# Performance work log

Measured on AMD Instinct MI355X. Metric: run time of the kernel, lower is better.

Reference implementation:

```python
import jax, jax.numpy as jnp
import numpy as np

F0, F1 = 10, 10  # num_neighbor_list fanouts
B = 4096         # sampled pos+neg edges


def setup_inputs() -> dict:
    key = jax.random.key(0)
    ks = jax.random.split(key, 24)
    def rn(k, shp, scale=0.05):
        return (jax.random.normal(k, shp, dtype=jnp.float32) * scale)
    inp = {
        "user_feat": rn(ks[0], (50000, 512), 1.0),
        "item_feat": rn(ks[1], (100000, 512), 1.0),
        "W_pu": rn(ks[2], (512, 256)), "b_pu": jnp.zeros((256,), jnp.float32),
        "W_pi": rn(ks[3], (512, 256)), "b_pi": jnp.zeros((256,), jnp.float32),
        "u_self0": rn(ks[4], (256, 256)), "u_agg0": rn(ks[5], (256, 256)),
        "u_self1": rn(ks[6], (256, 128)), "u_agg1": rn(ks[7], (256, 128)),
        "i_self0": rn(ks[8], (256, 256)), "i_agg0": rn(ks[9], (256, 256)),
        "i_self1": rn(ks[10], (256, 128)), "i_agg1": rn(ks[11], (256, 128)),
        "W_lin": rn(ks[12], (128, 1)), "b_lin": jnp.zeros((1,), jnp.float32),
        # precomputed multi-hop sampled node ids (alternating user/item spaces)
        "src_h0": jax.random.randint(ks[13], (B,), 0, 50000, dtype=jnp.int32),
        "src_h1": jax.random.randint(ks[14], (B * F0,), 0, 100000, dtype=jnp.int32),
        "src_h2": jax.random.randint(ks[15], (B * F0 * F1,), 0, 50000, dtype=jnp.int32),
        "dst_h0": jax.random.randint(ks[16], (B,), 0, 100000, dtype=jnp.int32),
        "dst_h1": jax.random.randint(ks[17], (B * F0,), 0, 50000, dtype=jnp.int32),
        "dst_h2": jax.random.randint(ks[18], (B * F0 * F1,), 0, 100000, dtype=jnp.int32),
    }
    return inp


def _sage(h0, h1, h2, Wself0, Wagg0, Wself1, Wagg1):
    # 2-layer GraphSAGE with mean aggregation over fixed fanouts.
    d = h0.shape[-1]
    # layer 0: update hop-0 and hop-1 representations
    n0 = h1.reshape(h0.shape[0], F0, d).mean(axis=1)          # [B, d]
    g0 = jax.nn.relu(h0 @ Wself0 + n0 @ Wagg0)                # [B, H0]
    n1 = h2.reshape(h1.shape[0], F1, d).mean(axis=1)          # [B*F0, d]
    g1 = jax.nn.relu(h1 @ Wself0 + n1 @ Wagg0)                # [B*F0, H0]
    # layer 1: final hop-0 representation (no activation on last layer)
    n = g1.reshape(g0.shape[0], F0, -1).mean(axis=1)          # [B, H0]
    return g0 @ Wself1 + n @ Wagg1                            # [B, H1]


def reference(user_feat, item_feat, W_pu, b_pu, W_pi, b_pi,
              u_self0, u_agg0, u_self1, u_agg1,
              i_self0, i_agg0, i_self1, i_agg1,
              W_lin, b_lin,
              src_h0, src_h1, src_h2, dst_h0, dst_h1, dst_h2):
    u_proj = jax.nn.sigmoid(user_feat @ W_pu + b_pu)   # [U, P]
    i_proj = jax.nn.sigmoid(item_feat @ W_pi + b_pi)   # [I, P]
    # src side alternates user/item per hop; dst side alternates item/user
    user_h = _sage(u_proj[src_h0], i_proj[src_h1], u_proj[src_h2],
                   u_self0, u_agg0, u_self1, u_agg1)
    item_h = _sage(i_proj[dst_h0], u_proj[dst_h1], i_proj[dst_h2],
                   i_self0, i_agg0, i_self1, i_agg1)
    logits = (user_h * item_h) @ W_lin + b_lin          # [B, 1]
    return logits
```

## Files before the change

kernel.cpp:

```cpp
#include <hip/hip_runtime.h>
#include <hip/hip_bf16.h>
#include <type_traits>

typedef __attribute__((ext_vector_type(8))) short short8;
typedef __attribute__((ext_vector_type(4))) float f32x4;
typedef unsigned short u16;
typedef unsigned int u32;

typedef const __attribute__((address_space(1))) u32* gp1_t;
typedef __attribute__((address_space(3))) u32* lp3_t;

__device__ __forceinline__ float bf2f(u16 u) {
    union { unsigned int i; float f; } x; x.i = ((unsigned int)u) << 16; return x.f;
}
__device__ __forceinline__ u16 f2bf(float f) {
    union { __hip_bfloat16 h; u16 u; } c; c.h = __float2bfloat16(f); return c.u;
}
__device__ __forceinline__ short8 cvt8(float4 v0, float4 v1) {
    union { u16 u[8]; short8 s; } p;
    p.u[0] = f2bf(v0.x); p.u[1] = f2bf(v0.y); p.u[2] = f2bf(v0.z); p.u[3] = f2bf(v0.w);
    p.u[4] = f2bf(v1.x); p.u[5] = f2bf(v1.y); p.u[6] = f2bf(v1.z); p.u[7] = f2bf(v1.w);
    return p.s;
}
__device__ __forceinline__ void gload_lds16(const void* g, void* l) {
    __builtin_amdgcn_global_load_lds((gp1_t)g, (lp3_t)l, 16, 0, 0);
}

struct TCJobs {
    const float* A[6];
    const float* Bm[6];
    u16* out[6];
    int N[6];
    int Ka[6];
};

__global__ void transcat6_k(TCJobs j) {
    int jid = blockIdx.y;
    int i = blockIdx.x * 256 + threadIdx.x;
    int N = j.N[jid];
    if (i >= N * 512) return;
    int n = i >> 9, k = i & 511, Ka = j.Ka[jid];
    float v = (k < Ka) ? j.A[jid][k * N + n] : j.Bm[jid][(k - Ka) * N + n];
    j.out[jid][i] = f2bf(v);
}

struct GJob {
    const void* A;
    const u16* WT;
    const float* bias;
    void* C;
    int M;
    int toff;
};
struct GJobs4 { GJob j[4]; };

template <int NJ, int WC, bool F32A, int ACT, bool OF32>
__global__ __launch_bounds__(WC * 128, 4) void gemm_k(GJobs4 js) {
    const int K = 512;
    const int N = WC * 64;
    __shared__ __align__(1024) char As[F32A ? 16384 : 8192];
    __shared__ __align__(1024) char Bs[WC * 4096];
    const int t = threadIdx.x;
    const int lane = t & 63;
    const int wid = t >> 6;
    const int wr = wid / WC, wc = wid % WC;
    const int lr = lane & 15;

    const int nwg = gridDim.x, p = blockIdx.x;
    const int q = nwg >> 3, rr = nwg & 7;
    const int xcd = p & 7, idx = p >> 3;
    const int L = (xcd < rr ? xcd * (q + 1) : rr * (q + 1) + (xcd - rr) * q) + idx;

    GJob jb = js.j[0];
    #pragma unroll
    for (int k = 1; k < NJ; ++k) if (L >= js.j[k].toff) jb = js.j[k];
    const int row_base = (L - jb.toff) * 128;
    const int M = jb.M;

    f32x4 acc[4][4] = {};

    for (int kt = 0; kt < K; kt += 32) {
        #pragma unroll
        for (int i = 0; i < 2; ++i) {
            int slot = wid * 2 + i;
            int rl = slot * 16 + (lane >> 2);
            int cc = (lane & 3) ^ ((rl >> 1) & 3);
            gload_lds16(&jb.WT[(size_t)rl * K + kt + cc * 8], &Bs[slot * 1024]);
        }
        if constexpr (F32A) {
            #pragma unroll
            for (int i = 0; i < 16 / (2 * WC); ++i) {
                int slot = wid * (16 / (2 * WC)) + i;
                int rl = slot * 8 + (lane >> 3);
                int sc = (lane & 7) ^ (rl & 7);
                int gr = row_base + rl; if (gr >= M) gr = M - 1;
                gload_lds16(&((const float*)jb.A)[(size_t)gr * K + kt + sc * 4],
                            &As[slot * 1024]);
            }
        } else {
            #pragma unroll
            for (int i = 0; i < 8 / (2 * WC); ++i) {
                int slot = wid * (8 / (2 * WC)) + i;
                int rl = slot * 16 + (lane >> 2);
                int cc = (lane & 3) ^ ((rl >> 1) & 3);
                int gr = row_base + rl; if (gr >= M) gr = M - 1;
                gload_lds16(&((const u16*)jb.A)[(size_t)gr * K + kt + cc * 8],
                            &As[slot * 1024]);
            }
        }
        __syncthreads();

        {
            const int g = lane >> 4;
            short8 a[4], b[4];
            #pragma unroll
            for (int ni = 0; ni < 4; ++ni) {
                int r = wc * 64 + ni * 16 + lr;
                b[ni] = *(const short8*)&Bs[r * 64 + ((g ^ ((r >> 1) & 3)) * 16)];
            }
            #pragma unroll
            for (int mi = 0; mi < 4; ++mi) {
                int r = wr * 64 + mi * 16 + lr;
                if constexpr (F32A) {
                    float4 v0 = *(const float4*)&As[r * 128 + (((2 * g) ^ (r & 7)) * 16)];
                    float4 v1 = *(const float4*)&As[r * 128 + (((2 * g + 1) ^ (r & 7)) * 16)];
                    a[mi] = cvt8(v0, v1);
                } else {
                    a[mi] = *(const short8*)&As[r * 64 + ((g ^ ((r >> 1) & 3)) * 16)];
                }
            }
            #pragma unroll
            for (int mi = 0; mi < 4; ++mi)
                #pragma unroll
                for (int ni = 0; ni < 4; ++ni)
                    acc[mi][ni] = __builtin_amdgcn_mfma_f32_16x16x32_bf16(
                        a[mi], b[ni], acc[mi][ni], 0, 0, 0);
        }
        __syncthreads();
    }

    #pragma unroll
    for (int mi = 0; mi < 4; ++mi) {
        int row0 = row_base + wr * 64 + mi * 16 + ((lane >> 4) << 2);
        #pragma unroll
        for (int ni = 0; ni < 4; ++ni) {
            int col = wc * 64 + ni * 16 + lr;
            float bv = jb.bias ? jb.bias[col] : 0.f;
            #pragma unroll
            for (int r = 0; r < 4; ++r) {
                int row = row0 + r;
                if (row < M) {
                    float x = acc[mi][ni][r] + bv;
                    if (ACT == 1) x = fmaxf(x, 0.f);
                    if (ACT == 2) x = 1.f / (1.f + __expf(-x));
                    if constexpr (OF32)
                        ((float*)jb.C)[(size_t)row * N + col] = x;
                    else
                        ((u16*)jb.C)[(size_t)row * N + col] = f2bf(x);
                }
            }
        }
    }
}

struct FJob {
    const u16* G0;
    const u16* G1;
    const u16* WT;
    float* C;
    int toff;
};
struct FJobs2 { FJob j[2]; };

__global__ __launch_bounds__(256, 4) void final_k(FJobs2 js) {
    const int K = 512;
    __shared__ __align__(1024) char As[8192];
    __shared__ __align__(1024) char Bs[8192];
    const int t = threadIdx.x;
    const int lane = t & 63;
    const int wid = t >> 6;
    const int wr = wid >> 1, wc = wid & 1;
    const int lr = lane & 15;

    const int L = blockIdx.x;
    FJob jb = js.j[0];
    if (L >= js.j[1].toff) jb = js.j[1];
    const int row_base = (L - jb.toff) * 128;

    f32x4 acc[4][4] = {};

    for (int kt = 0; kt < K; kt += 32) {
        #pragma unroll
        for (int i = 0; i < 2; ++i) {
            int slot = wid * 2 + i;
            int rl = slot * 16 + (lane >> 2);
            int cc = (lane & 3) ^ ((rl >> 1) & 3);
            gload_lds16(&jb.WT[(size_t)rl * K + kt + cc * 8], &Bs[slot * 1024]);
        }
        if (kt < 256) {
            #pragma unroll
            for (int i = 0; i < 2; ++i) {
                int slot = wid * 2 + i;
                int rl = slot * 16 + (lane >> 2);
                int cc = (lane & 3) ^ ((rl >> 1) & 3);
                gload_lds16(&jb.G0[(size_t)(row_base + rl) * 256 + kt + cc * 8],
                            &As[slot * 1024]);
            }
        } else {
            #pragma unroll
            for (int u = 0; u < 2; ++u) {
                int unit = u * 256 + t;
                int r = unit >> 2, c8 = unit & 3;
                int col = (kt - 256) + c8 * 8;
                const u16* g1 = &jb.G1[(size_t)(row_base + r) * 10 * 256 + col];
                float s[8] = {};
                #pragma unroll
                for (int f = 0; f < 10; ++f) {
                    short8 nv = *(const short8*)&g1[(size_t)f * 256];
                    #pragma unroll
                    for (int jj = 0; jj < 8; ++jj) s[jj] += bf2f((u16)nv[jj]);
                }
                union { u16 uu[8]; short8 v; } o;
                #pragma unroll
                for (int jj = 0; jj < 8; ++jj) o.uu[jj] = f2bf(s[jj] * 0.1f);
                *(short8*)&As[r * 64 + ((c8 ^ ((r >> 1) & 3)) * 16)] = o.v;
            }
        }
        __syncthreads();

        {
            const int g = lane >> 4;
            short8 a[4], b[4];
            #pragma unroll
            for (int ni = 0; ni < 4; ++ni) {
                int r = wc * 64 + ni * 16 + lr;
                b[ni] = *(const short8*)&Bs[r * 64 + ((g ^ ((r >> 1) & 3)) * 16)];
            }
            #pragma unroll
            for (int mi = 0; mi < 4; ++mi) {
                int r = wr * 64 + mi * 16 + lr;
                a[mi] = *(const short8*)&As[r * 64 + ((g ^ ((r >> 1) & 3)) * 16)];
            }
            #pragma unroll
            for (int mi = 0; mi < 4; ++mi)
                #pragma unroll
                for (int ni = 0; ni < 4; ++ni)
                    acc[mi][ni] = __builtin_amdgcn_mfma_f32_16x16x32_bf16(
                        a[mi], b[ni], acc[mi][ni], 0, 0, 0);
        }
        __syncthreads();
    }

    #pragma unroll
    for (int mi = 0; mi < 4; ++mi) {
        int row0 = row_base + wr * 64 + mi * 16 + ((lane >> 4) << 2);
        #pragma unroll
        for (int ni = 0; ni < 4; ++ni) {
            int col = wc * 64 + ni * 16 + lr;
            #pragma unroll
            for (int r = 0; r < 4; ++r)
                jb.C[(size_t)(row0 + r) * 128 + col] = acc[mi][ni][r];
        }
    }
}

struct BJob {
    u16* X;
    const u16* selfP;
    const int* sidx;
    const u16* nbP;
    const int* nidx;
    int roff;
};
struct BJobs4 { BJob j[4]; };

template <int NJ>
__global__ void build_xm_k(BJobs4 bj, int total) {
    int gw = (int)((blockIdx.x * blockDim.x + threadIdx.x) >> 5);
    int hl = threadIdx.x & 31;
    if (gw >= total) return;
    BJob jb = bj.j[0];
    #pragma unroll
    for (int k = 1; k < NJ; ++k) if (gw >= bj.j[k].roff) jb = bj.j[k];
    int r = gw - jb.roff;

    int c8 = hl * 8;
    int sr = jb.sidx ? jb.sidx[r] : r;
    short8 sv = *(const short8*)&jb.selfP[(size_t)sr * 256 + c8];
    *(short8*)&jb.X[(size_t)r * 512 + c8] = sv;

    float s[8] = {};
    #pragma unroll
    for (int f = 0; f < 10; ++f) {
        int nr = jb.nidx ? jb.nidx[r * 10 + f] : r * 10 + f;
        short8 nv = *(const short8*)&jb.nbP[(size_t)nr * 256 + c8];
        #pragma unroll
        for (int jj = 0; jj < 8; ++jj) s[jj] += bf2f((u16)nv[jj]);
    }
    union { u16 u[8]; short8 v; } o;
    #pragma unroll
    for (int jj = 0; jj < 8; ++jj) o.u[jj] = f2bf(s[jj] * 0.1f);
    *(short8*)&jb.X[(size_t)r * 512 + 256 + c8] = o.v;
}

__global__ void logits_k(const float* __restrict__ hu, const float* __restrict__ hi,
                         const float* __restrict__ wlin, const float* __restrict__ blin,
                         float* __restrict__ out, int Bn) {
    int w = (blockIdx.x * blockDim.x + threadIdx.x) >> 6;
    int lane = threadIdx.x & 63;
    if (w >= Bn) return;
    float s = 0.f;
    #pragma unroll
    for (int k = lane; k < 128; k += 64)
        s += hu[(size_t)w * 128 + k] * hi[(size_t)w * 128 + k] * wlin[k];
    #pragma unroll
    for (int off = 32; off > 0; off >>= 1) s += __shfl_down(s, off, 64);
    if (lane == 0) out[w] = s + blin[0];
}

extern "C" void kernel_launch(void* const* d_in, const int* in_sizes, int n_in,
                              void* d_out, int out_size, void* d_ws, size_t ws_size,
                              hipStream_t stream) {
    const float* user_feat = (const float*)d_in[0];
    const float* item_feat = (const float*)d_in[1];
    const float* W_pu = (const float*)d_in[2];
    const float* b_pu = (const float*)d_in[3];
    const float* W_pi = (const float*)d_in[4];
    const float* b_pi = (const float*)d_in[5];
    const float* u_self0 = (const float*)d_in[6];
    const float* u_agg0 = (const float*)d_in[7];
    const float* u_self1 = (const float*)d_in[8];
    const float* u_agg1 = (const float*)d_in[9];
    const float* i_self0 = (const float*)d_in[10];
    const float* i_agg0 = (const float*)d_in[11];
    const float* i_self1 = (const float*)d_in[12];
    const float* i_agg1 = (const float*)d_in[13];
    const float* W_lin = (const float*)d_in[14];
    const float* b_lin = (const float*)d_in[15];
    const int* src_h0 = (const int*)d_in[16];
    const int* src_h1 = (const int*)d_in[17];
    const int* src_h2 = (const int*)d_in[18];
    const int* dst_h0 = (const int*)d_in[19];
    const int* dst_h1 = (const int*)d_in[20];
    const int* dst_h2 = (const int*)d_in[21];
    float* out = (float*)d_out;

    const int NU = 50000, NI = 100000, B = 4096, BF = 40960;

    char* ws = (char*)d_ws;
    size_t off = 0;
    auto alloc = [&](size_t bytes) -> void* {
        void* p = ws + off;
        off += (bytes + 255) & ~(size_t)255;
        return p;
    };
    u16* Pu   = (u16*)alloc((size_t)NU * 256 * 2);
    u16* Pi   = (u16*)alloc((size_t)NI * 256 * 2);
    u16* X1a  = (u16*)alloc((size_t)BF * 512 * 2);
    u16* X1b  = (u16*)alloc((size_t)BF * 512 * 2);
    u16* G1a  = (u16*)alloc((size_t)BF * 256 * 2);
    u16* G1b  = (u16*)alloc((size_t)BF * 256 * 2);
    u16* X0a  = (u16*)alloc((size_t)B * 512 * 2);
    u16* X0b  = (u16*)alloc((size_t)B * 512 * 2);
    u16* G0a  = (u16*)alloc((size_t)B * 256 * 2);
    u16* G0b  = (u16*)alloc((size_t)B * 256 * 2);
    float* Hu = (float*)alloc((size_t)B * 128 * 4);
    float* Hi = (float*)alloc((size_t)B * 128 * 4);
    u16* WpuT = (u16*)alloc(256 * 512 * 2);
    u16* WpiT = (u16*)alloc(256 * 512 * 2);
    u16* W0uT = (u16*)alloc(256 * 512 * 2);
    u16* W0iT = (u16*)alloc(256 * 512 * 2);
    u16* W1uT = (u16*)alloc(128 * 512 * 2);
    u16* W1iT = (u16*)alloc(128 * 512 * 2);

    TCJobs tj;
    tj.A[0] = W_pu;    tj.Bm[0] = W_pu;    tj.out[0] = WpuT; tj.N[0] = 256; tj.Ka[0] = 512;
    tj.A[1] = W_pi;    tj.Bm[1] = W_pi;    tj.out[1] = WpiT; tj.N[1] = 256; tj.Ka[1] = 512;
    tj.A[2] = u_self0; tj.Bm[2] = u_agg0;  tj.out[2] = W0uT; tj.N[2] = 256; tj.Ka[2] = 256;
    tj.A[3] = i_self0; tj.Bm[3] = i_agg0;  tj.out[3] = W0iT; tj.N[3] = 256; tj.Ka[3] = 256;
    tj.A[4] = u_self1; tj.Bm[4] = u_agg1;  tj.out[4] = W1uT; tj.N[4] = 128; tj.Ka[4] = 256;
    tj.A[5] = i_self1; tj.Bm[5] = i_agg1;  tj.out[5] = W1iT; tj.N[5] = 128; tj.Ka[5] = 256;
    transcat6_k<<<dim3(512, 6), 256, 0, stream>>>(tj);

    const int ptu = (NU + 127) / 128;
    const int pti = (NI + 127) / 128;
    GJobs4 pj;
    pj.j[0] = {user_feat, WpuT, b_pu, Pu, NU, 0};
    pj.j[1] = {item_feat, WpiT, b_pi, Pi, NI, ptu};
    pj.j[2] = pj.j[1]; pj.j[3] = pj.j[1];
    gemm_k<2, 4, true, 2, false><<<ptu + pti, 512, 0, stream>>>(pj);

    BJobs4 b1;
    b1.j[0] = {X1a, Pi, src_h1, Pu, src_h2, 0};
    b1.j[1] = {X1b, Pu, dst_h1, Pi, dst_h2, BF};
    b1.j[2] = {X0a, Pu, src_h0, Pi, src_h1, 2 * BF};
    b1.j[3] = {X0b, Pi, dst_h0, Pu, dst_h1, 2 * BF + B};
    const int tot1 = 2 * BF + 2 * B;
    build_xm_k<4><<<tot1 / 8, 256, 0, stream>>>(b1, tot1);

    GJobs4 sj;
    sj.j[0] = {X1a, W0uT, nullptr, G1a, BF, 0};
    sj.j[1] = {X1b, W0iT, nullptr, G1b, BF, 320};
    sj.j[2] = {X0a, W0uT, nullptr, G0a, B, 640};
    sj.j[3] = {X0b, W0iT, nullptr, G0b, B, 672};
    gemm_k<4, 4, false, 1, false><<<704, 512, 0, stream>>>(sj);

    FJobs2 fj;
    fj.j[0] = {G0a, G1a, W1uT, Hu, 0};
    fj.j[1] = {G0b, G1b, W1iT, Hi, 32};
    final_k<<<64, 256, 0, stream>>>(fj);

    logits_k<<<B / 4, 256, 0, stream>>>(Hu, Hi, W_lin, b_lin, out, B);
}
```

Baseline: 309.6 us.

## Fuse neighbor gather and mean aggregation into the layer-0 SAGE GEMM

Removes the separate build kernel that materialized the concatenated [self | mean-neighbor] X matrices in global memory, and instead gathers and averages neighbor rows directly into LDS A-tiles inside a new GEMM kernel. This eliminates writing and re-reading roughly 88 MB of intermediate X buffers and one kernel launch. The trade-off is that the irregular gather with 10 dependent loads per element now sits on the GEMM's critical path. Each K-step reloads the index arrays, and there is no double buffering to hide the gather latency.

```diff
diff --git a/kernel.cpp b/kernel.cpp
--- a/kernel.cpp
+++ b/kernel.cpp
@@ -163,6 +163,112 @@
     }
 }
 
+struct SJob {
+    const u16* selfP;
+    const int* sidx;
+    const u16* nbP;
+    const int* nidx;
+    const u16* WT;
+    u16* C;
+    int M;
+    int toff;
+};
+struct SJobs4 { SJob j[4]; };
+
+__global__ __launch_bounds__(512, 4) void sage0_k(SJobs4 js) {
+    const int K = 512;
+    __shared__ __align__(1024) char As[8192];
+    __shared__ __align__(1024) char Bs[16384];
+    const int t = threadIdx.x;
+    const int lane = t & 63;
+    const int wid = t >> 6;
+    const int wr = wid >> 2, wc = wid & 3;
+    const int lr = lane & 15;
+
+    const int nwg = gridDim.x, p = blockIdx.x;
+    const int q = nwg >> 3, rr = nwg & 7;
+    const int xcd = p & 7, idx = p >> 3;
+    const int L = (xcd < rr ? xcd * (q + 1) : rr * (q + 1) + (xcd - rr) * q) + idx;
+
+    SJob jb = js.j[0];
+    #pragma unroll
+    for (int k = 1; k < 4; ++k) if (L >= js.j[k].toff) jb = js.j[k];
+    const int row_base = (L - jb.toff) * 128;
+
+    f32x4 acc[4][4] = {};
+
+    for (int kt = 0; kt < K; kt += 32) {
+        #pragma unroll
+        for (int i = 0; i < 2; ++i) {
+            int slot = wid * 2 + i;
+            int rl = slot * 16 + (lane >> 2);
+            int cc = (lane & 3) ^ ((rl >> 1) & 3);
+            gload_lds16(&jb.WT[(size_t)rl * K + kt + cc * 8], &Bs[slot * 1024]);
+        }
+        {
+            int r = t >> 2, c8 = t & 3;
+            int gr = row_base + r;
+            short8 v;
+            if (kt < 256) {
+                int sr = jb.sidx[gr];
+                v = *(const short8*)&jb.selfP[(size_t)sr * 256 + kt + c8 * 8];
+            } else {
+                int col = (kt - 256) + c8 * 8;
+                float s[8] = {};
+                #pragma unroll
+                for (int f = 0; f < 10; ++f) {
+                    int nr = jb.nidx[gr * 10 + f];
+                    short8 nv = *(const short8*)&jb.nbP[(size_t)nr * 256 + col];
+                    #pragma unroll
+                    for (int jj = 0; jj < 8; ++jj) s[jj] += bf2f((u16)nv[jj]);
+                }
+                union { u16 uu[8]; short8 vv; } o;
+                #pragma unroll
+                for (int jj = 0; jj < 8; ++jj) o.uu[jj] = f2bf(s[jj] * 0.1f);
+                v = o.vv;
+            }
+            *(short8*)&As[r * 64 + ((c8 ^ ((r >> 1) & 3)) * 16)] = v;
+        }
+        __syncthreads();
+
+        {
+            const int g = lane >> 4;
+            short8 a[4], b[4];
+            #pragma unroll
+            for (int ni = 0; ni < 4; ++ni) {
+                int r = wc * 64 + ni * 16 + lr;
+                b[ni] = *(const short8*)&Bs[r * 64 + ((g ^ ((r >> 1) & 3)) * 16)];
+            }
+            #pragma unroll
+            for (int mi = 0; mi < 4; ++mi) {
+                int r = wr * 64 + mi * 16 + lr;
+                a[mi] = *(const short8*)&As[r * 64 + ((g ^ ((r >> 1) & 3)) * 16)];
+            }
+            #pragma unroll
+            for (int mi = 0; mi < 4; ++mi)
+                #pragma unroll
+                for (int ni = 0; ni < 4; ++ni)
+                    acc[mi][ni] = __builtin_amdgcn_mfma_f32_16x16x32_bf16(
+                        a[mi], b[ni], acc[mi][ni], 0, 0, 0);
+        }
+        __syncthreads();
+    }
+
+    #pragma unroll
+    for (int mi = 0; mi < 4; ++mi) {
+        int row0 = row_base + wr * 64 + mi * 16 + ((lane >> 4) << 2);
+        #pragma unroll
+        for (int ni = 0; ni < 4; ++ni) {
+            int col = wc * 64 + ni * 16 + lr;
+            #pragma unroll
+            for (int r = 0; r < 4; ++r) {
+                float x = fmaxf(acc[mi][ni][r], 0.f);
+                jb.C[(size_t)(row0 + r) * 256 + col] = f2bf(x);
+            }
+        }
+    }
+}
+
 struct FJob {
     const u16* G0;
     const u16* G1;
@@ -262,45 +368,6 @@
                 jb.C[(size_t)(row0 + r) * 128 + col] = acc[mi][ni][r];
         }
     }
-}
-
-struct BJob {
-    u16* X;
-    const u16* selfP;
-    const int* sidx;
-    const u16* nbP;
-    const int* nidx;
-    int roff;
-};
-struct BJobs4 { BJob j[4]; };
-
-template <int NJ>
-__global__ void build_xm_k(BJobs4 bj, int total) {
-    int gw = (int)((blockIdx.x * blockDim.x + threadIdx.x) >> 5);
-    int hl = threadIdx.x & 31;
-    if (gw >= total) return;
-    BJob jb = bj.j[0];
-    #pragma unroll
-    for (int k = 1; k < NJ; ++k) if (gw >= bj.j[k].roff) jb = bj.j[k];
-    int r = gw - jb.roff;
-
-    int c8 = hl * 8;
-    int sr = jb.sidx ? jb.sidx[r] : r;
-    short8 sv = *(const short8*)&jb.selfP[(size_t)sr * 256 + c8];
-    *(short8*)&jb.X[(size_t)r * 512 + c8] = sv;
-
-    float s[8] = {};
-    #pragma unroll
-    for (int f = 0; f < 10; ++f) {
-        int nr = jb.nidx ? jb.nidx[r * 10 + f] : r * 10 + f;
-        short8 nv = *(const short8*)&jb.nbP[(size_t)nr * 256 + c8];
-        #pragma unroll
-        for (int jj = 0; jj < 8; ++jj) s[jj] += bf2f((u16)nv[jj]);
-    }
-    union { u16 u[8]; short8 v; } o;
-    #pragma unroll
-    for (int jj = 0; jj < 8; ++jj) o.u[jj] = f2bf(s[jj] * 0.1f);
-    *(short8*)&jb.X[(size_t)r * 512 + 256 + c8] = o.v;
 }
 
 __global__ void logits_k(const float* __restrict__ hu, const float* __restrict__ hi,
@@ -356,12 +423,8 @@
     };
     u16* Pu   = (u16*)alloc((size_t)NU * 256 * 2);
     u16* Pi   = (u16*)alloc((size_t)NI * 256 * 2);
-    u16* X1a  = (u16*)alloc((size_t)BF * 512 * 2);
-    u16* X1b  = (u16*)alloc((size_t)BF * 512 * 2);
     u16* G1a  = (u16*)alloc((size_t)BF * 256 * 2);
     u16* G1b  = (u16*)alloc((size_t)BF * 256 * 2);
-    u16* X0a  = (u16*)alloc((size_t)B * 512 * 2);
-    u16* X0b  = (u16*)alloc((size_t)B * 512 * 2);
     u16* G0a  = (u16*)alloc((size_t)B * 256 * 2);
     u16* G0b  = (u16*)alloc((size_t)B * 256 * 2);
     float* Hu = (float*)alloc((size_t)B * 128 * 4);
@@ -390,20 +453,12 @@
     pj.j[2] = pj.j[1]; pj.j[3] = pj.j[1];
     gemm_k<2, 4, true, 2, false><<<ptu + pti, 512, 0, stream>>>(pj);
 
-    BJobs4 b1;
-    b1.j[0] = {X1a, Pi, src_h1, Pu, src_h2, 0};
-    b1.j[1] = {X1b, Pu, dst_h1, Pi, dst_h2, BF};
-    b1.j[2] = {X0a, Pu, src_h0, Pi, src_h1, 2 * BF};
-    b1.j[3] = {X0b, Pi, dst_h0, Pu, dst_h1, 2 * BF + B};
-    const int tot1 = 2 * BF + 2 * B;
-    build_xm_k<4><<<tot1 / 8, 256, 0, stream>>>(b1, tot1);
-
-    GJobs4 sj;
-    sj.j[0] = {X1a, W0uT, nullptr, G1a, BF, 0};
-    sj.j[1] = {X1b, W0iT, nullptr, G1b, BF, 320};
-    sj.j[2] = {X0a, W0uT, nullptr, G0a, B, 640};
-    sj.j[3] = {X0b, W0iT, nullptr, G0b, B, 672};
-    gemm_k<4, 4, false, 1, false><<<704, 512, 0, stream>>>(sj);
+    SJobs4 sj;
+    sj.j[0] = {Pi, src_h1, Pu, src_h2, W0uT, G1a, BF, 0};
+    sj.j[1] = {Pu, dst_h1, Pi, dst_h2, W0iT, G1b, BF, 320};
+    sj.j[2] = {Pu, src_h0, Pi, src_h1, W0uT, G0a, B, 640};
+    sj.j[3] = {Pi, dst_h0, Pu, dst_h1, W0iT, G0b, B, 672};
+    sage0_k<<<704, 512, 0, stream>>>(sj);
 
     FJobs2 fj;
     fj.j[0] = {G0a, G1a, W1uT, Hu, 0};
```

New measurement: 322.7 us. 4.3% more time.
